# Optimization experiments

Measured on AMD Instinct MI355X. Metric: run time of the kernel, lower is better.

## Reference

```python
import jax, jax.numpy as jnp
import numpy as np

B, T, C = 4, 2048, 1024
H = 16
D = C // H  # 64

def setup_inputs() -> dict:
    key = jax.random.key(0)
    k1, k2, k3, k4, k5 = jax.random.split(key, 5)
    s = 0.02
    return {
        "x": jax.random.normal(k1, (B, T, C), dtype=jnp.float32),
        "Wqkv": jax.random.normal(k2, (C, 3 * C), dtype=jnp.float32) * s,
        "bqkv": jnp.zeros((3 * C,), dtype=jnp.float32),
        "Wout": jax.random.normal(k3, (C, C), dtype=jnp.float32) * s,
        "bout": jnp.zeros((C,), dtype=jnp.float32),
    }

def reference(x, Wqkv, bqkv, Wout, bout):
    b, t, c = x.shape
    scale = D ** -0.5
    qkv = x @ Wqkv + bqkv                      # [B,T,3C]
    qkv = qkv.reshape(b, t, 3, H, D)
    q = qkv[:, :, 0].transpose(0, 2, 1, 3)     # [B,H,T,D]
    k = qkv[:, :, 1].transpose(0, 2, 1, 3)
    v = qkv[:, :, 2].transpose(0, 2, 1, 3)
    att = jnp.einsum('bhqd,bhkd->bhqk', q, k) * scale
    causal = jnp.tril(jnp.ones((t, t), dtype=bool))
    att = jnp.where(causal, att, -jnp.inf)
    att = jax.nn.softmax(att, axis=-1)
    y = jnp.einsum('bhqk,bhkd->bhqd', att, v)  # [B,H,T,D]
    y = y.transpose(0, 2, 1, 3).reshape(b, t, c)
    return y @ Wout + bout
```

## Files before the change

kernel.cpp:

```cpp
#include <hip/hip_runtime.h>
#include <hip/hip_bf16.h>


using f32x4 = __attribute__((ext_vector_type(4))) float;
using s16x8 = __attribute__((ext_vector_type(8))) short;
using s16x4 = __attribute__((ext_vector_type(4))) short;

#define MFMA16(a, b, c) __builtin_amdgcn_mfma_f32_16x16x32_bf16(a, b, c, 0, 0, 0)

__device__ __forceinline__ unsigned short f2bf(float f) {
    unsigned u = __builtin_bit_cast(unsigned, f);
    u += 0x7fffu + ((u >> 16) & 1u);
    return (unsigned short)(u >> 16);
}

__device__ __forceinline__ void gl_lds16(const void* g, void* l) {
    __builtin_amdgcn_global_load_lds(
        (const __attribute__((address_space(1))) void*)g,
        (__attribute__((address_space(3))) void*)l, 16, 0, 0);
}

__global__ __launch_bounds__(256) void cvt_x(const float* __restrict__ x,
                                             unsigned short* __restrict__ xb, int n4) {
    int i = blockIdx.x * 256 + threadIdx.x;
    if (i < n4) {
        f32x4 v = ((const f32x4*)x)[i];
        s16x4 o;
        o[0] = (short)f2bf(v[0]); o[1] = (short)f2bf(v[1]);
        o[2] = (short)f2bf(v[2]); o[3] = (short)f2bf(v[3]);
        ((s16x4*)xb)[i] = o;
    }
}

__global__ __launch_bounds__(256) void cvt_tr(const float* __restrict__ W,
                                              unsigned short* __restrict__ Wt,
                                              int R, int Cc) {
    __shared__ unsigned short tile[64][72];
    const int r0 = blockIdx.x * 64, c0 = blockIdx.y * 64;
    const int tid = threadIdx.x;
    const int r = tid >> 4, c4 = (tid & 15) * 4;
#pragma unroll
    for (int i = 0; i < 4; ++i) {
        f32x4 v = *(const f32x4*)(W + (size_t)(r0 + r + i * 16) * Cc + c0 + c4);
#pragma unroll
        for (int j = 0; j < 4; ++j) tile[r + i * 16][c4 + j] = f2bf(v[j]);
    }
    __syncthreads();
#pragma unroll
    for (int i = 0; i < 4; ++i) {
        s16x4 o;
#pragma unroll
        for (int j = 0; j < 4; ++j) o[j] = (short)tile[c4 + j][r + i * 16];
        *(s16x4*)(Wt + (size_t)(c0 + r + i * 16) * R + r0 + c4) = o;
    }
}

template <int MODE>
__global__ __launch_bounds__(256, 2) void gemm_bt(
    const unsigned short* __restrict__ A, const unsigned short* __restrict__ Bt,
    const float* __restrict__ bias,
    unsigned short* __restrict__ qp, unsigned short* __restrict__ kp,
    unsigned short* __restrict__ vtp, float* __restrict__ outp,
    int M, int N, int K)
{
    __shared__ unsigned short As[2][128 * 64];
    __shared__ unsigned short Bs[2][128 * 64];

    const int tid  = threadIdx.x;
    const int lane = tid & 63, w = tid >> 6;
    const int wm = w >> 1, wn = w & 1;
    const int g = lane >> 4, li = lane & 15;
    const int m0 = blockIdx.x * 128, n0 = blockIdx.y * 128;

    const int srow = lane >> 3;
    const int ssw  = ((lane & 7) ^ srow) * 8;

    f32x4 acc[4][4] = {};

    auto STAGE = [&](int buf, int k0) {
#pragma unroll
        for (int j = 0; j < 4; ++j) {
            const int rr = w * 32 + j * 8;
            gl_lds16(A  + (size_t)(m0 + rr + srow) * K + k0 + ssw, &As[buf][rr * 64]);
            gl_lds16(Bt + (size_t)(n0 + rr + srow) * K + k0 + ssw, &Bs[buf][rr * 64]);
        }
    };

    STAGE(0, 0);
    asm volatile("s_waitcnt vmcnt(0)" ::: "memory");
    __syncthreads();

    const int nt = K >> 6;
    int cur = 0;
    for (int t = 0; t < nt; ++t) {
        if (t + 1 < nt) STAGE(cur ^ 1, (t + 1) << 6);

        s16x8 af[4][2], bf[4][2];
#pragma unroll
        for (int i = 0; i < 4; ++i) {
            const int ra = wm * 64 + i * 16 + li;
            const int rb = wn * 64 + i * 16 + li;
#pragma unroll
            for (int kk = 0; kk < 2; ++kk) {
                af[i][kk] = *(const s16x8*)(
                    &As[cur][ra * 64 + (((kk * 4 + g) ^ (ra & 7)) << 3)]);
                bf[i][kk] = *(const s16x8*)(
                    &Bs[cur][rb * 64 + (((kk * 4 + g) ^ (rb & 7)) << 3)]);
            }
        }

        __builtin_amdgcn_s_setprio(1);
#pragma unroll
        for (int kk = 0; kk < 2; ++kk)
#pragma unroll
            for (int mi = 0; mi < 4; ++mi)
#pragma unroll
                for (int ni = 0; ni < 4; ++ni)
                    acc[mi][ni] = MFMA16(af[mi][kk], bf[ni][kk], acc[mi][ni]);
        __builtin_amdgcn_s_setprio(0);

        asm volatile("s_waitcnt vmcnt(0)" ::: "memory");
        __syncthreads();
        cur ^= 1;
    }

#pragma unroll
    for (int ni = 0; ni < 4; ++ni) {
        const int n = n0 + wn * 64 + ni * 16 + li;
        const float bv = bias[n];
        const int s = n >> 10, h = (n >> 6) & 15, d = n & 63;
#pragma unroll
        for (int mi = 0; mi < 4; ++mi) {
            const int mB = m0 + wm * 64 + mi * 16 + g * 4;
            float v0 = acc[mi][ni][0] + bv, v1 = acc[mi][ni][1] + bv;
            float v2 = acc[mi][ni][2] + bv, v3 = acc[mi][ni][3] + bv;
            if (MODE == 0) {
                const int b = mB >> 11, tt = mB & 2047;
                if (s == 2) {
                    unsigned pk01, pk23;
                    asm("v_cvt_pk_bf16_f32 %0, %1, %2" : "=v"(pk01) : "v"(v0), "v"(v1));
                    asm("v_cvt_pk_bf16_f32 %0, %1, %2" : "=v"(pk23) : "v"(v2), "v"(v3));
                    unsigned short* dst = vtp + ((size_t)(b * 16 + h) * 64 + d) * 2048 + tt;
                    *(unsigned*)dst = pk01;
                    *(unsigned*)(dst + 2) = pk23;
                } else {
                    const float sc2 = (s == 0) ? 0.1803368801111143f : 1.0f;
                    unsigned short* dst =
                        ((s == 0) ? qp : kp) + ((size_t)(b * 16 + h) * 2048 + tt) * 64 + d;
                    dst[0]   = f2bf(v0 * sc2);
                    dst[64]  = f2bf(v1 * sc2);
                    dst[128] = f2bf(v2 * sc2);
                    dst[192] = f2bf(v3 * sc2);
                }
            } else {
                float* dst = outp + (size_t)mB * N + n;
                dst[0] = v0; dst[N] = v1; dst[2 * N] = v2; dst[3 * N] = v3;
            }
        }
    }
}

__device__ __forceinline__ void stage_kv(
    const unsigned short* __restrict__ kb, const unsigned short* __restrict__ vtb,
    unsigned short* KsB, unsigned short* VsB, int kbase, int w, int lane)
{
    const int srow = lane >> 3;
    const int sw = ((lane & 7) ^ srow) * 8;
#pragma unroll
    for (int jj = 0; jj < 2; ++jj) {
        const int j = w * 2 + jj;
        const int row = j * 8 + srow;
        gl_lds16(kb  + (size_t)(kbase + row) * 64 + sw, KsB + j * 512);
        gl_lds16(vtb + (size_t)row * 2048 + kbase + sw, VsB + j * 512);
    }
}

__device__ __forceinline__ void qk_softmax(
    const unsigned short* Ks, const s16x8 qf0, const s16x8 qf1,
    f32x4 (&O)[4], float& m, float& l,
    unsigned short (*Psw)[72], s16x8& pf0, s16x8& pf1,
    int kbase, int wq0, int qrow, int g, int li)
{
    f32x4 sT[4];
    __builtin_amdgcn_s_setprio(1);
#pragma unroll
    for (int nf = 0; nf < 4; ++nf) {
        const int r = nf * 16 + li;
        s16x8 kf0 = *(const s16x8*)(Ks + r * 64 + ((g ^ (li & 7)) << 3));
        s16x8 kf1 = *(const s16x8*)(Ks + r * 64 + (((g + 4) ^ (li & 7)) << 3));
        f32x4 a = {};
        a = MFMA16(kf0, qf0, a);
        a = MFMA16(kf1, qf1, a);
        sT[nf] = a;
    }
    __builtin_amdgcn_s_setprio(0);

    if (kbase + 63 > wq0) {
#pragma unroll
        for (int nf = 0; nf < 4; ++nf)
#pragma unroll
            for (int r = 0; r < 4; ++r)
                if (kbase + nf * 16 + g * 4 + r > qrow) sT[nf][r] = -1e30f;
    }

    float t0 = fmaxf(fmaxf(sT[0][0], sT[0][1]), sT[0][2]);
    float t1 = fmaxf(fmaxf(sT[0][3], sT[1][0]), sT[1][1]);
    float t2 = fmaxf(fmaxf(sT[1][2], sT[1][3]), sT[2][0]);
    float t3 = fmaxf(fmaxf(sT[2][1], sT[2][2]), sT[2][3]);
    float t4 = fmaxf(fmaxf(sT[3][0], sT[3][1]), sT[3][2]);
    float mx = fmaxf(fmaxf(t0, t1), t2);
    mx = fmaxf(fmaxf(mx, t3), fmaxf(t4, sT[3][3]));
    mx = fmaxf(mx, __shfl_xor(mx, 16));
    mx = fmaxf(mx, __shfl_xor(mx, 32));

    if (__any(mx > m + 8.f)) {
        const float mnew = fmaxf(m, mx);
        const float fac  = __builtin_amdgcn_exp2f(m - mnew);
        m = mnew;
        l *= fac;
        float facr[4];
#pragma unroll
        for (int r = 0; r < 4; ++r) facr[r] = __shfl(fac, g * 4 + r);
#pragma unroll
        for (int nf = 0; nf < 4; ++nf)
#pragma unroll
            for (int r = 0; r < 4; ++r) O[nf][r] *= facr[r];
    }

    float rs = 0.f;
#pragma unroll
    for (int nf = 0; nf < 4; ++nf)
#pragma unroll
        for (int r = 0; r < 4; ++r) {
            float p = __builtin_amdgcn_exp2f(sT[nf][r] - m);
            sT[nf][r] = p;
            rs += p;
        }
    rs += __shfl_xor(rs, 16);
    rs += __shfl_xor(rs, 32);
    l += rs;

#pragma unroll
    for (int nf = 0; nf < 4; ++nf) {
        unsigned pk0, pk1;
        asm("v_cvt_pk_bf16_f32 %0, %1, %2" : "=v"(pk0) : "v"(sT[nf][0]), "v"(sT[nf][1]));
        asm("v_cvt_pk_bf16_f32 %0, %1, %2" : "=v"(pk1) : "v"(sT[nf][2]), "v"(sT[nf][3]));
        uint2 pv; pv.x = pk0; pv.y = pk1;
        *(uint2*)(&Psw[li][nf * 16 + g * 4]) = pv;
    }
    pf0 = *(const s16x8*)(&Psw[li][g * 8]);
    pf1 = *(const s16x8*)(&Psw[li][32 + g * 8]);
}

__global__ __launch_bounds__(256, 4) void attn_k(
    const unsigned short* __restrict__ qbuf,
    const unsigned short* __restrict__ kbuf,
    const unsigned short* __restrict__ vtbuf,
    unsigned short* __restrict__ ybuf)
{
    __shared__ unsigned short Ks[4096];
    __shared__ unsigned short Vs[4096];
    __shared__ unsigned short PsA[4][16][72];
    __shared__ unsigned short PsB[4][16][72];

    const int tid  = threadIdx.x;
    const int lane = tid & 63, w = tid >> 6;
    const int g = lane >> 4, li = lane & 15;

    const int id   = blockIdx.x;
    const int slot = id >> 3;
    const int bh   = (id & 7) * 8 + (slot & 7);
    const int bx   = slot >> 3;
    const int qtA  = 31 - bx, qtB = bx;

    const unsigned short* qb  = qbuf  + (size_t)bh * 131072;
    const unsigned short* kb  = kbuf  + (size_t)bh * 131072;
    const unsigned short* vtb = vtbuf + (size_t)bh * 131072;
    const int b = bh >> 4, h = bh & 15;

    const int wqA = qtA * 64 + w * 16, qrowA = wqA + li;
    const int wqB = qtB * 64 + w * 16, qrowB = wqB + li;

    const unsigned short* qrA = qb + (size_t)qrowA * 64 + g * 8;
    const s16x8 qfA0 = *(const s16x8*)qrA;
    const s16x8 qfA1 = *(const s16x8*)(qrA + 32);
    const unsigned short* qrB = qb + (size_t)qrowB * 64 + g * 8;
    const s16x8 qfB0 = *(const s16x8*)qrB;
    const s16x8 qfB1 = *(const s16x8*)(qrB + 32);

    f32x4 OA[4] = {}, OB[4] = {};
    float mA = -1e30f, lA = 0.f, mB = -1e30f, lB = 0.f;

    const int nkb = qtA + 1;
    stage_kv(kb, vtb, Ks, Vs, 0, w, lane);
    asm volatile("s_waitcnt vmcnt(0)" ::: "memory");
    __syncthreads();

    for (int t = 0; t < nkb; ++t) {
        const int kbase = t * 64;
        const bool actB = (t <= qtB);

        s16x8 pfA0, pfA1, pfB0, pfB1;
        qk_softmax(Ks, qfA0, qfA1, OA, mA, lA, &PsA[w][0], pfA0, pfA1,
                   kbase, wqA, qrowA, g, li);
        if (actB)
            qk_softmax(Ks, qfB0, qfB1, OB, mB, lB, &PsB[w][0], pfB0, pfB1,
                       kbase, wqB, qrowB, g, li);

        __builtin_amdgcn_s_setprio(1);
#pragma unroll
        for (int nf = 0; nf < 4; ++nf) {
            const int d = nf * 16 + li;
            s16x8 vf0 = *(const s16x8*)(Vs + d * 64 + ((g ^ (li & 7)) << 3));
            s16x8 vf1 = *(const s16x8*)(Vs + d * 64 + (((g + 4) ^ (li & 7)) << 3));
            OA[nf] = MFMA16(pfA0, vf0, OA[nf]);
            OA[nf] = MFMA16(pfA1, vf1, OA[nf]);
            if (actB) {
                OB[nf] = MFMA16(pfB0, vf0, OB[nf]);
                OB[nf] = MFMA16(pfB1, vf1, OB[nf]);
            }
        }
        __builtin_amdgcn_s_setprio(0);

        if (t + 1 < nkb) {
            __syncthreads();
            stage_kv(kb, vtb, Ks, Vs, kbase + 64, w, lane);
            asm volatile("s_waitcnt vmcnt(0)" ::: "memory");
            __syncthreads();
        }
    }

    {
        const float linv = __builtin_amdgcn_rcpf(lA);
        float lr[4];
#pragma unroll
        for (int r = 0; r < 4; ++r) lr[r] = __shfl(linv, g * 4 + r);
#pragma unroll
        for (int nf = 0; nf < 4; ++nf)
#pragma unroll
            for (int r = 0; r < 4; ++r) {
                const int row = wqA + g * 4 + r;
                ybuf[((size_t)(b * 2048 + row)) * 1024 + h * 64 + nf * 16 + li] =
                    f2bf(OA[nf][r] * lr[r]);
            }
    }
    {
        const float linv = __builtin_amdgcn_rcpf(lB);
        float lr[4];
#pragma unroll
        for (int r = 0; r < 4; ++r) lr[r] = __shfl(linv, g * 4 + r);
#pragma unroll
        for (int nf = 0; nf < 4; ++nf)
#pragma unroll
            for (int r = 0; r < 4; ++r) {
                const int row = wqB + g * 4 + r;
                ybuf[((size_t)(b * 2048 + row)) * 1024 + h * 64 + nf * 16 + li] =
                    f2bf(OB[nf][r] * lr[r]);
            }
    }
}

extern "C" void kernel_launch(void* const* d_in, const int* in_sizes, int n_in,
                              void* d_out, int out_size, void* d_ws, size_t ws_size,
                              hipStream_t stream)
{
    const float* x    = (const float*)d_in[0];
    const float* Wqkv = (const float*)d_in[1];
    const float* bqkv = (const float*)d_in[2];
    const float* Wout = (const float*)d_in[3];
    const float* bout = (const float*)d_in[4];

    unsigned short* ws0 = (unsigned short*)d_ws;
    unsigned short* ws1 = ws0 + (size_t)8388608;
    unsigned short* ws2 = ws0 + (size_t)2 * 8388608;
    unsigned short* ws3 = ws0 + (size_t)3 * 8388608;

    unsigned short* xbf   = (unsigned short*)d_out;
    unsigned short* WqkvT = xbf + (size_t)8388608;

    cvt_x<<<8192, 256, 0, stream>>>(x, xbf, 2097152);
    cvt_tr<<<dim3(16, 48), 256, 0, stream>>>(Wqkv, WqkvT, 1024, 3072);
    gemm_bt<0><<<dim3(64, 24), 256, 0, stream>>>(
        xbf, WqkvT, bqkv, ws0, ws1, ws2, nullptr, 8192, 3072, 1024);
    attn_k<<<1024, 256, 0, stream>>>(ws0, ws1, ws2, ws3);
    cvt_tr<<<dim3(16, 16), 256, 0, stream>>>(Wout, ws0, 1024, 1024);
    gemm_bt<1><<<dim3(64, 8), 256, 0, stream>>>(
        ws3, ws0, bout, nullptr, nullptr, nullptr, (float*)d_out, 8192, 1024, 1024);
}
```

Measured before the change: 167.9 us.

## Prefetch next K/V tile into registers during compute instead of direct-to-LDS loads

```diff
diff --git a/kernel.cpp b/kernel.cpp
--- a/kernel.cpp
+++ b/kernel.cpp
@@ -160,18 +160,29 @@
     }
 }
 
-__device__ __forceinline__ void stage_kv(
+__device__ __forceinline__ void stage_load(
     const unsigned short* __restrict__ kb, const unsigned short* __restrict__ vtb,
-    unsigned short* KsB, unsigned short* VsB, int kbase, int w, int lane)
+    int kbase, int w, int lane, s16x8 (&kr)[2], s16x8 (&vr)[2])
 {
     const int srow = lane >> 3;
     const int sw = ((lane & 7) ^ srow) * 8;
 #pragma unroll
     for (int jj = 0; jj < 2; ++jj) {
+        const int row = (w * 2 + jj) * 8 + srow;
+        kr[jj] = *(const s16x8*)(kb + (size_t)(kbase + row) * 64 + sw);
+        vr[jj] = *(const s16x8*)(vtb + (size_t)row * 2048 + kbase + sw);
+    }
+}
+
+__device__ __forceinline__ void stage_write(
+    unsigned short* Ks, unsigned short* Vs, int w, int lane,
+    const s16x8 (&kr)[2], const s16x8 (&vr)[2])
+{
+#pragma unroll
+    for (int jj = 0; jj < 2; ++jj) {
         const int j = w * 2 + jj;
-        const int row = j * 8 + srow;
-        gl_lds16(kb  + (size_t)(kbase + row) * 64 + sw, KsB + j * 512);
-        gl_lds16(vtb + (size_t)row * 2048 + kbase + sw, VsB + j * 512);
+        *(s16x8*)(Ks + j * 512 + lane * 8) = kr[jj];
+        *(s16x8*)(Vs + j * 512 + lane * 8) = vr[jj];
     }
 }
 
@@ -260,8 +271,7 @@
 {
     __shared__ unsigned short Ks[4096];
     __shared__ unsigned short Vs[4096];
-    __shared__ unsigned short PsA[4][16][72];
-    __shared__ unsigned short PsB[4][16][72];
+    __shared__ unsigned short Ps[4][16][72];
 
     const int tid  = threadIdx.x;
     const int lane = tid & 63, w = tid >> 6;
@@ -292,19 +302,23 @@
     float mA = -1e30f, lA = 0.f, mB = -1e30f, lB = 0.f;
 
     const int nkb = qtA + 1;
-    stage_kv(kb, vtb, Ks, Vs, 0, w, lane);
-    asm volatile("s_waitcnt vmcnt(0)" ::: "memory");
+    s16x8 kr[2], vr[2];
+    stage_load(kb, vtb, 0, w, lane, kr, vr);
+    stage_write(Ks, Vs, w, lane, kr, vr);
     __syncthreads();
 
     for (int t = 0; t < nkb; ++t) {
         const int kbase = t * 64;
         const bool actB = (t <= qtB);
+        const bool more = (t + 1 < nkb);
+
+        if (more) stage_load(kb, vtb, kbase + 64, w, lane, kr, vr);
 
         s16x8 pfA0, pfA1, pfB0, pfB1;
-        qk_softmax(Ks, qfA0, qfA1, OA, mA, lA, &PsA[w][0], pfA0, pfA1,
+        qk_softmax(Ks, qfA0, qfA1, OA, mA, lA, &Ps[w][0], pfA0, pfA1,
                    kbase, wqA, qrowA, g, li);
         if (actB)
-            qk_softmax(Ks, qfB0, qfB1, OB, mB, lB, &PsB[w][0], pfB0, pfB1,
+            qk_softmax(Ks, qfB0, qfB1, OB, mB, lB, &Ps[w][0], pfB0, pfB1,
                        kbase, wqB, qrowB, g, li);
 
         __builtin_amdgcn_s_setprio(1);
@@ -322,10 +336,9 @@
         }
         __builtin_amdgcn_s_setprio(0);
 
-        if (t + 1 < nkb) {
+        if (more) {
             __syncthreads();
-            stage_kv(kb, vtb, Ks, Vs, kbase + 64, w, lane);
-            asm volatile("s_waitcnt vmcnt(0)" ::: "memory");
+            stage_write(Ks, Vs, w, lane, kr, vr);
             __syncthreads();
         }
     }
```

New measurement: 178.3 us. +6.2%, slower.
